# Kernel optimization log

Hardware: AMD Instinct MI355X
Metric: run time of the kernel (lower is better)

## Reference

```python
import jax, jax.numpy as jnp
import numpy as np

DEGREE = 3
N_KNOTS = 5

def _bspline_basis(x, t_ext, degree):
    """Vectorized Cox-de Boor. x: (..., ), t_ext: (m,) extended knots.
    Returns (..., m-1-degree) degree-`degree` basis values."""
    xe = x[..., None]
    # order-0 indicator basis: (..., m-1)
    B = ((xe >= t_ext[:-1]) & (xe < t_ext[1:])).astype(x.dtype)
    for p in range(1, degree + 1):
        left_den = t_ext[p:-1] - t_ext[:-(p + 1)]
        right_den = t_ext[p + 1:] - t_ext[1:-p]
        left = jnp.where(left_den > 0,
                         (xe - t_ext[:-(p + 1)]) / jnp.where(left_den > 0, left_den, 1.0),
                         0.0) * B[..., :-1]
        right = jnp.where(right_den > 0,
                          (t_ext[p + 1:] - xe) / jnp.where(right_den > 0, right_den, 1.0),
                          0.0) * B[..., 1:]
        B = left + right
    return B

def setup_inputs() -> dict:
    key = jax.random.key(0)
    k1, k2, k3, k4 = jax.random.split(key, 4)
    batch, input_dim, out_dim = 16384, 4096, 64
    n_coeff = N_KNOTS - DEGREE  # 2
    return {
        "x": jax.random.normal(k1, (batch, input_dim), dtype=jnp.float32),
        "c": jax.random.normal(k2, (input_dim, out_dim, n_coeff), dtype=jnp.float32),
        "ws": jax.random.normal(k3, (input_dim, out_dim), dtype=jnp.float32),
        "wb": jax.random.normal(k4, (input_dim, out_dim), dtype=jnp.float32),
    }

def reference(x, c, ws, wb):
    t = jnp.linspace(-1.0, 1.0, N_KNOTS, dtype=x.dtype)
    t_ext = jnp.concatenate([t, t[-1:]])  # pad so basis count == n_knots - degree
    # B: (batch, input_dim, n_coeff); basis depends only on x, shared knots
    B = _bspline_basis(x, t_ext, DEGREE)
    spline = jnp.einsum('bik,ijk->bj', B, c * ws[:, :, None])
    silu_mix = jax.nn.silu(x) @ wb  # sum_i wb[i,j] * x_i*sigmoid(x_i)
    return spline + silu_mix
```

## Files before the change

### kernel.cpp

```cpp
#include <hip/hip_runtime.h>
#include <hip/hip_bf16.h>
#include <stdint.h>

#define BATCH   16384
#define IN_DIM  4096
#define OUT_DIM 64
#define KI      64
#define KCH     (3*KI)
#define NCHUNK  (IN_DIM/KI)
#define SPLITK  4
#define CPB     (NCHUNK/SPLITK)
#define MTILES  (BATCH/64)
#define CHW     (OUT_DIM*KCH)

typedef __attribute__((ext_vector_type(8))) short   short8;
typedef __attribute__((ext_vector_type(4))) float   floatx4;
typedef __attribute__((ext_vector_type(4))) uint32_t uintx4;

static __device__ __forceinline__ unsigned short f2bf(float f) {
    union { float f; uint32_t u; } v; v.f = f;
    uint32_t r = v.u + 0x7FFFu + ((v.u >> 16) & 1u);
    return (unsigned short)(r >> 16);
}

static __device__ __forceinline__ void kan_features(float xv, float& b0, float& b1, float& sl) {
    float ax = fabsf(xv);
    float a2 = ax*ax;
    float om = 1.0f - ax;
    float inner = __builtin_fmaf(__builtin_fmaf(4.0f, ax, -4.0f), a2, (2.0f/3.0f));
    float outer = (om*om) * (om * (4.0f/3.0f));
    b0 = (ax < 0.5f) ? inner : outer;
    b0 = (ax < 1.0f) ? b0 : 0.0f;
    float c3  = (xv < 0.0f) ? (4.0f/3.0f) : (-14.0f/3.0f);
    float mid = __builtin_fmaf(__builtin_fmaf(__builtin_fmaf(c3, xv, 2.0f), xv, 1.0f), xv, (1.0f/6.0f));
    float hi  = __builtin_fmaf(__builtin_fmaf(__builtin_fmaf(22.0f, xv, -48.0f), xv, 30.0f), xv, -4.0f) * (1.0f/3.0f);
    b1 = (xv < 0.5f) ? mid : hi;
    b1 = (xv >= -0.5f && xv < 1.0f) ? b1 : 0.0f;
    float e = __expf(-xv);
    sl = xv * __builtin_amdgcn_rcpf(1.0f + e);
}

__global__ __launch_bounds__(256) void kan_prep(
        const float* __restrict__ c, const float* __restrict__ ws,
        const float* __restrict__ wb, unsigned short* __restrict__ Wt) {
    int idx = blockIdx.x * 256 + threadIdx.x;
    int row = idx >> 9;
    int i   = (idx & 511) << 3;
    int j   = row / 3;
    int t   = row - j*3;
    int ci  = i >> 6, il0 = i & 63;
    unsigned short pk[8];
    #pragma unroll
    for (int e = 0; e < 8; e++) {
        int ii = i + e;
        float v;
        if (t < 2) v = c[(size_t)ii*(OUT_DIM*2) + j*2 + t] * ws[(size_t)ii*OUT_DIM + j];
        else       v = wb[(size_t)ii*OUT_DIM + j];
        pk[e] = f2bf(v);
    }
    uintx4 d;
    d[0] = pk[0] | ((uint32_t)pk[1] << 16);
    d[1] = pk[2] | ((uint32_t)pk[3] << 16);
    d[2] = pk[4] | ((uint32_t)pk[5] << 16);
    d[3] = pk[6] | ((uint32_t)pk[7] << 16);
    int g = j*24 + (((t << 3) | (il0 >> 3)) ^ (j & 7));
    *(uintx4*)(Wt + (size_t)ci*CHW + g*8) = d;
}

template<bool PRE>
__global__ __launch_bounds__(256, 4) void kan_main(
    const float* __restrict__ x, const float* __restrict__ c,
    const float* __restrict__ ws, const float* __restrict__ wb,
    const unsigned short* __restrict__ Wt, float* __restrict__ out)
{
    __shared__ unsigned short Bs[CHW];

    const int tid  = threadIdx.x;
    const int wave = tid >> 6;
    const int lane = tid & 63;
    const int m    = lane & 15;
    const int q    = lane >> 4;
    const int mt   = blockIdx.x & (MTILES - 1);
    const int kh   = blockIdx.x >> 8;
    const int row0 = mt * 64;
    const int r    = row0 + wave*16 + m;
    const float* xrow = x + (size_t)r * IN_DIM;

    floatx4 acc[4] = {};

    const int i00 = kh * CPB * KI;
    floatx4 xv[4];
    xv[0] = *(const floatx4*)(xrow + i00 + q*8);
    xv[1] = *(const floatx4*)(xrow + i00 + q*8 + 4);
    xv[2] = *(const floatx4*)(xrow + i00 + 32 + q*8);
    xv[3] = *(const floatx4*)(xrow + i00 + 32 + q*8 + 4);

    for (int cc = 0; cc < CPB; cc++) {
        const int ci = kh * CPB + cc;
        const int i0 = ci * KI;

        uintx4 stg[6];
        if (PRE) {
            const unsigned short* gW = Wt + (size_t)ci * CHW;
            #pragma unroll
            for (int p = 0; p < 6; p++)
                stg[p] = *(const uintx4*)(gW + (tid + p*256)*8);
        }

        const int inx = (cc + 1 < CPB) ? (i0 + KI) : i0;
        floatx4 xvn[4];
        xvn[0] = *(const floatx4*)(xrow + inx + q*8);
        xvn[1] = *(const floatx4*)(xrow + inx + q*8 + 4);
        xvn[2] = *(const floatx4*)(xrow + inx + 32 + q*8);
        xvn[3] = *(const floatx4*)(xrow + inx + 32 + q*8 + 4);

        short8 af[6];
        #pragma unroll
        for (int g = 0; g < 2; g++) {
            #pragma unroll
            for (int e = 0; e < 8; e++) {
                float v = xv[g*2 + (e >> 2)][e & 3];
                float b0, b1, sl;
                kan_features(v, b0, b1, sl);
                af[0 + g][e] = (short)f2bf(b0);
                af[2 + g][e] = (short)f2bf(b1);
                af[4 + g][e] = (short)f2bf(sl);
            }
        }

        __syncthreads();

        if (PRE) {
            #pragma unroll
            for (int p = 0; p < 6; p++)
                *(uintx4*)&Bs[(tid + p*256)*8] = stg[p];
        } else {
            #pragma unroll
            for (int p = 0; p < 16; p++) {
                int idx = tid + p*256;
                int j = idx & 63, i = idx >> 6;
                int gi = i0 + i;
                const float* cp = c + ((size_t)gi*OUT_DIM + j)*2;
                float c0 = cp[0], c1 = cp[1];
                float s  = ws[(size_t)gi*OUT_DIM + j];
                float b  = wb[(size_t)gi*OUT_DIM + j];
                int jx = j & 7;
                Bs[j*KCH + ((0*8 + (i>>3)) ^ jx)*8 + (i&7)] = f2bf(c0*s);
                Bs[j*KCH + ((1*8 + (i>>3)) ^ jx)*8 + (i&7)] = f2bf(c1*s);
                Bs[j*KCH + ((2*8 + (i>>3)) ^ jx)*8 + (i&7)] = f2bf(b);
            }
        }

        __syncthreads();

        #pragma unroll
        for (int s = 0; s < 6; s++) {
            const int kb = (s >> 1)*8 + (s & 1)*4 + q;
            #pragma unroll
            for (int n = 0; n < 4; n++) {
                const int j = n*16 + m;
                short8 bf = *(const short8*)&Bs[j*KCH + ((kb ^ (j & 7)) << 3)];
                acc[n] = __builtin_amdgcn_mfma_f32_16x16x32_bf16(af[s], bf, acc[n], 0, 0, 0);
            }
        }

        xv[0] = xvn[0]; xv[1] = xvn[1]; xv[2] = xvn[2]; xv[3] = xvn[3];
    }

    #pragma unroll
    for (int n = 0; n < 4; n++) {
        #pragma unroll
        for (int reg = 0; reg < 4; reg++) {
            int orow = row0 + wave*16 + q*4 + reg;
            atomicAdd(&out[(size_t)orow*OUT_DIM + n*16 + m], acc[n][reg]);
        }
    }
}

extern "C" void kernel_launch(void* const* d_in, const int* in_sizes, int n_in,
                              void* d_out, int out_size, void* d_ws, size_t ws_size,
                              hipStream_t stream) {
    const float* x  = (const float*)d_in[0];
    const float* c  = (const float*)d_in[1];
    const float* ws = (const float*)d_in[2];
    const float* wb = (const float*)d_in[3];
    float* out = (float*)d_out;

    hipMemsetAsync(d_out, 0, (size_t)out_size * sizeof(float), stream);

    const size_t need = (size_t)NCHUNK * CHW * sizeof(unsigned short);
    if (ws_size >= need) {
        kan_prep<<<384, 256, 0, stream>>>(c, ws, wb, (unsigned short*)d_ws);
        kan_main<true><<<MTILES * SPLITK, 256, 0, stream>>>(
            x, c, ws, wb, (const unsigned short*)d_ws, out);
    } else {
        kan_main<false><<<MTILES * SPLITK, 256, 0, stream>>>(
            x, c, ws, wb, (const unsigned short*)d_ws, out);
    }
}
```

Before: 403.5 us.

## Load weights via global_load_lds, replace atomics with split-K partial buffer reduce

Weight chunks now move from global memory straight into LDS through global_load_lds, with no register staging. The split-K atomicAdd epilogue and the output memset are replaced by partial-sum stores to a workspace buffer, followed by a separate reduce kernel. The bf16 conversion now packs two values per 32-bit word. The changes target register pressure, atomic contention and memset cost, at the price of an extra kernel launch, about 16MB of partial-buffer traffic, and a larger workspace requirement.

New measurement: 411.3 us. About the same (+1.9%).

```diff
diff --git a/kernel.cpp b/kernel.cpp
--- a/kernel.cpp
+++ b/kernel.cpp
@@ -21,6 +21,14 @@
     union { float f; uint32_t u; } v; v.f = f;
     uint32_t r = v.u + 0x7FFFu + ((v.u >> 16) & 1u);
     return (unsigned short)(r >> 16);
+}
+
+static __device__ __forceinline__ uint32_t pk2bf(float lo, float hi) {
+    union { float f; uint32_t u; } a, b;
+    a.f = lo; b.f = hi;
+    uint32_t ra = a.u + 0x7FFFu + ((a.u >> 16) & 1u);
+    uint32_t rb = b.u + 0x7FFFu + ((b.u >> 16) & 1u);
+    return (ra >> 16) | (rb & 0xFFFF0000u);
 }
 
 static __device__ __forceinline__ void kan_features(float xv, float& b0, float& b1, float& sl) {
@@ -67,11 +75,9 @@
     *(uintx4*)(Wt + (size_t)ci*CHW + g*8) = d;
 }
 
-template<bool PRE>
-__global__ __launch_bounds__(256, 4) void kan_main(
-    const float* __restrict__ x, const float* __restrict__ c,
-    const float* __restrict__ ws, const float* __restrict__ wb,
-    const unsigned short* __restrict__ Wt, float* __restrict__ out)
+__global__ __launch_bounds__(256, 4) void kan_main_pre(
+    const float* __restrict__ x, const unsigned short* __restrict__ Wt,
+    float* __restrict__ pbuf)
 {
     __shared__ unsigned short Bs[CHW];
 
@@ -99,14 +105,6 @@
         const int ci = kh * CPB + cc;
         const int i0 = ci * KI;
 
-        uintx4 stg[6];
-        if (PRE) {
-            const unsigned short* gW = Wt + (size_t)ci * CHW;
-            #pragma unroll
-            for (int p = 0; p < 6; p++)
-                stg[p] = *(const uintx4*)(gW + (tid + p*256)*8);
-        }
-
         const int inx = (cc + 1 < CPB) ? (i0 + KI) : i0;
         floatx4 xvn[4];
         xvn[0] = *(const floatx4*)(xrow + inx + q*8);
@@ -114,41 +112,32 @@
         xvn[2] = *(const floatx4*)(xrow + inx + 32 + q*8);
         xvn[3] = *(const floatx4*)(xrow + inx + 32 + q*8 + 4);
 
-        short8 af[6];
+        uintx4 afu[6];
         #pragma unroll
         for (int g = 0; g < 2; g++) {
             #pragma unroll
-            for (int e = 0; e < 8; e++) {
-                float v = xv[g*2 + (e >> 2)][e & 3];
-                float b0, b1, sl;
-                kan_features(v, b0, b1, sl);
-                af[0 + g][e] = (short)f2bf(b0);
-                af[2 + g][e] = (short)f2bf(b1);
-                af[4 + g][e] = (short)f2bf(sl);
-            }
-        }
-
-        __syncthreads();
-
-        if (PRE) {
-            #pragma unroll
-            for (int p = 0; p < 6; p++)
-                *(uintx4*)&Bs[(tid + p*256)*8] = stg[p];
-        } else {
-            #pragma unroll
-            for (int p = 0; p < 16; p++) {
-                int idx = tid + p*256;
-                int j = idx & 63, i = idx >> 6;
-                int gi = i0 + i;
-                const float* cp = c + ((size_t)gi*OUT_DIM + j)*2;
-                float c0 = cp[0], c1 = cp[1];
-                float s  = ws[(size_t)gi*OUT_DIM + j];
-                float b  = wb[(size_t)gi*OUT_DIM + j];
-                int jx = j & 7;
-                Bs[j*KCH + ((0*8 + (i>>3)) ^ jx)*8 + (i&7)] = f2bf(c0*s);
-                Bs[j*KCH + ((1*8 + (i>>3)) ^ jx)*8 + (i&7)] = f2bf(c1*s);
-                Bs[j*KCH + ((2*8 + (i>>3)) ^ jx)*8 + (i&7)] = f2bf(b);
-            }
+            for (int w = 0; w < 4; w++) {
+                float v0 = xv[g*2 + (w >> 1)][(w & 1)*2 + 0];
+                float v1 = xv[g*2 + (w >> 1)][(w & 1)*2 + 1];
+                float b00, b10, sl0, b01, b11, sl1;
+                kan_features(v0, b00, b10, sl0);
+                kan_features(v1, b01, b11, sl1);
+                afu[0 + g][w] = pk2bf(b00, b01);
+                afu[2 + g][w] = pk2bf(b10, b11);
+                afu[4 + g][w] = pk2bf(sl0, sl1);
+            }
+        }
+
+        __syncthreads();
+
+        const unsigned short* gW = Wt + (size_t)ci * CHW;
+        #pragma unroll
+        for (int p = 0; p < 6; p++) {
+            int g0 = p*256 + wave*64;
+            __builtin_amdgcn_global_load_lds(
+                (__attribute__((address_space(1))) void*)(gW + (size_t)(g0 + lane)*8),
+                (__attribute__((address_space(3))) void*)(Bs + (size_t)g0*8),
+                16, 0, 0);
         }
 
         __syncthreads();
@@ -160,21 +149,120 @@
             for (int n = 0; n < 4; n++) {
                 const int j = n*16 + m;
                 short8 bf = *(const short8*)&Bs[j*KCH + ((kb ^ (j & 7)) << 3)];
-                acc[n] = __builtin_amdgcn_mfma_f32_16x16x32_bf16(af[s], bf, acc[n], 0, 0, 0);
+                acc[n] = __builtin_amdgcn_mfma_f32_16x16x32_bf16(
+                    __builtin_bit_cast(short8, afu[s]), bf, acc[n], 0, 0, 0);
             }
         }
 
         xv[0] = xvn[0]; xv[1] = xvn[1]; xv[2] = xvn[2]; xv[3] = xvn[3];
     }
 
+    float* pb = pbuf + (((size_t)kh*MTILES + mt)*4)*256*4;
+    #pragma unroll
+    for (int n = 0; n < 4; n++)
+        *(floatx4*)(pb + ((size_t)n*256 + tid)*4) = acc[n];
+}
+
+__global__ __launch_bounds__(256) void kan_reduce(
+    const float* __restrict__ pbuf, float* __restrict__ out)
+{
+    const int mt   = blockIdx.x;
+    const int tid  = threadIdx.x;
+    const int wave = tid >> 6;
+    const int lane = tid & 63;
+    const int m    = lane & 15;
+    const int q    = lane >> 4;
     #pragma unroll
     for (int n = 0; n < 4; n++) {
+        floatx4 s = {};
+        #pragma unroll
+        for (int p = 0; p < SPLITK; p++) {
+            floatx4 v = *(const floatx4*)(pbuf +
+                ((((size_t)p*MTILES + mt)*4 + n)*256 + tid)*4);
+            s += v;
+        }
+        #pragma unroll
+        for (int reg = 0; reg < 4; reg++) {
+            int orow = mt*64 + wave*16 + q*4 + reg;
+            out[(size_t)orow*OUT_DIM + n*16 + m] = s[reg];
+        }
+    }
+}
+
+__global__ __launch_bounds__(256, 4) void kan_main_fb(
+    const float* __restrict__ x, const float* __restrict__ c,
+    const float* __restrict__ ws, const float* __restrict__ wb,
+    float* __restrict__ out)
+{
+    __shared__ unsigned short Bs[CHW];
+    const int tid  = threadIdx.x;
+    const int wave = tid >> 6;
+    const int lane = tid & 63;
+    const int m    = lane & 15;
+    const int q    = lane >> 4;
+    const int mt   = blockIdx.x & (MTILES - 1);
+    const int kh   = blockIdx.x >> 8;
+    const int row0 = mt * 64;
+    const int r    = row0 + wave*16 + m;
+    const float* xrow = x + (size_t)r * IN_DIM;
+    floatx4 acc[4] = {};
+    for (int cc = 0; cc < CPB; cc++) {
+        const int i0 = (kh * CPB + cc) * KI;
+        floatx4 xv[4];
+        xv[0] = *(const floatx4*)(xrow + i0 + q*8);
+        xv[1] = *(const floatx4*)(xrow + i0 + q*8 + 4);
+        xv[2] = *(const floatx4*)(xrow + i0 + 32 + q*8);
+        xv[3] = *(const floatx4*)(xrow + i0 + 32 + q*8 + 4);
+        uintx4 afu[6];
+        #pragma unroll
+        for (int g = 0; g < 2; g++) {
+            #pragma unroll
+            for (int w = 0; w < 4; w++) {
+                float v0 = xv[g*2 + (w >> 1)][(w & 1)*2 + 0];
+                float v1 = xv[g*2 + (w >> 1)][(w & 1)*2 + 1];
+                float b00, b10, sl0, b01, b11, sl1;
+                kan_features(v0, b00, b10, sl0);
+                kan_features(v1, b01, b11, sl1);
+                afu[0 + g][w] = pk2bf(b00, b01);
+                afu[2 + g][w] = pk2bf(b10, b11);
+                afu[4 + g][w] = pk2bf(sl0, sl1);
+            }
+        }
+        __syncthreads();
+        #pragma unroll
+        for (int p = 0; p < 16; p++) {
+            int idx = tid + p*256;
+            int j = idx & 63, i = idx >> 6;
+            int gi = i0 + i;
+            const float* cp = c + ((size_t)gi*OUT_DIM + j)*2;
+            float c0 = cp[0], c1 = cp[1];
+            float sw = ws[(size_t)gi*OUT_DIM + j];
+            float b  = wb[(size_t)gi*OUT_DIM + j];
+            int jx = j & 7;
+            Bs[j*KCH + ((0*8 + (i>>3)) ^ jx)*8 + (i&7)] = f2bf(c0*sw);
+            Bs[j*KCH + ((1*8 + (i>>3)) ^ jx)*8 + (i&7)] = f2bf(c1*sw);
+            Bs[j*KCH + ((2*8 + (i>>3)) ^ jx)*8 + (i&7)] = f2bf(b);
+        }
+        __syncthreads();
+        #pragma unroll
+        for (int s = 0; s < 6; s++) {
+            const int kb = (s >> 1)*8 + (s & 1)*4 + q;
+            #pragma unroll
+            for (int n = 0; n < 4; n++) {
+                const int j = n*16 + m;
+                short8 bf = *(const short8*)&Bs[j*KCH + ((kb ^ (j & 7)) << 3)];
+                acc[n] = __builtin_amdgcn_mfma_f32_16x16x32_bf16(
+                    __builtin_bit_cast(short8, afu[s]), bf, acc[n], 0, 0, 0);
+            }
+        }
+    }
+    #pragma unroll
+    for (int n = 0; n < 4; n++)
         #pragma unroll
         for (int reg = 0; reg < 4; reg++) {
             int orow = row0 + wave*16 + q*4 + reg;
             atomicAdd(&out[(size_t)orow*OUT_DIM + n*16 + m], acc[n][reg]);
         }
-    }
 }
 
 extern "C" void kernel_launch(void* const* d_in, const int* in_sizes, int n_in,
@@ -186,15 +274,16 @@
     const float* wb = (const float*)d_in[3];
     float* out = (float*)d_out;
 
-    hipMemsetAsync(d_out, 0, (size_t)out_size * sizeof(float), stream);
-
-    const size_t need = (size_t)NCHUNK * CHW * sizeof(unsigned short);
-    if (ws_size >= need) {
-        kan_prep<<<384, 256, 0, stream>>>(c, ws, wb, (unsigned short*)d_ws);
-        kan_main<true><<<MTILES * SPLITK, 256, 0, stream>>>(
-            x, c, ws, wb, (const unsigned short*)d_ws, out);
+    const size_t part_bytes = (size_t)SPLITK * BATCH * OUT_DIM * sizeof(float);
+    const size_t wt_bytes   = (size_t)NCHUNK * CHW * sizeof(unsigned short);
+    if (ws_size >= part_bytes + wt_bytes) {
+        float* pbuf = (float*)d_ws;
+        unsigned short* Wt = (unsigned short*)((char*)d_ws + part_bytes);
+        kan_prep<<<384, 256, 0, stream>>>(c, ws, wb, Wt);
+        kan_main_pre<<<MTILES * SPLITK, 256, 0, stream>>>(x, Wt, pbuf);
+        kan_reduce<<<MTILES, 256, 0, stream>>>(pbuf, out);
     } else {
-        kan_main<false><<<MTILES * SPLITK, 256, 0, stream>>>(
-            x, c, ws, wb, (const unsigned short*)d_ws, out);
-    }
-}
+        hipMemsetAsync(d_out, 0, (size_t)out_size * sizeof(float), stream);
+        kan_main_fb<<<MTILES * SPLITK, 256, 0, stream>>>(x, c, ws, wb, out);
+    }
+}
```
